# Performance work log

Measured on AMD Instinct MI355X. Metric: run time of the kernel, lower is better.

The kernel has to match this reference:

```python
import jax, jax.numpy as jnp
import numpy as np

B, L, D_IN, D_MODEL, D_STATE, D_DISCR, KER = 2, 1024, 512, 1024, 16, 64, 4


def setup_inputs() -> dict:
    ks = jax.random.split(jax.random.key(0), 9)
    s = 0.02
    return {
        "seq": jax.random.normal(ks[0], (B, L, D_IN), jnp.float32),
        "W_in": jax.random.normal(ks[1], (2 * D_MODEL, D_IN), jnp.float32) * s,
        "W_out": jax.random.normal(ks[2], (D_IN, D_MODEL), jnp.float32) * s,
        "W_B": jax.random.normal(ks[3], (D_STATE, D_MODEL), jnp.float32) * s,
        "W_C": jax.random.normal(ks[4], (D_STATE, D_MODEL), jnp.float32) * s,
        "W_D1": jax.random.normal(ks[5], (D_DISCR, D_MODEL), jnp.float32) * s,
        "W_D2": jax.random.normal(ks[6], (D_MODEL, D_DISCR), jnp.float32) * s,
        "conv_w": jax.random.normal(ks[7], (D_MODEL, 1, KER), jnp.float32) * 0.1,
        "conv_b": jax.random.normal(ks[8], (D_MODEL,), jnp.float32) * 0.01,
        "A": jnp.tile(jnp.arange(1, D_STATE + 1, dtype=jnp.float32), (D_MODEL, 1)),
        "D": jnp.ones((D_MODEL,), jnp.float32),
    }


def _causal_depthwise_conv(x, w, b):
    # x: [B, L, D] -> torch Conv1d(groups=D, padding=KER-1) truncated to first L outputs
    x = jnp.swapaxes(x, 1, 2)  # [B, D, L]
    y = jax.lax.conv_general_dilated(
        x, w, window_strides=(1,), padding=[(KER - 1, 0)],
        dimension_numbers=("NCH", "OIH", "NCH"), feature_group_count=D_MODEL)
    y = y + b[None, :, None]
    return jnp.swapaxes(y, 1, 2)  # [B, L, D]


def _ssm(x, W_B, W_C, W_D1, W_D2, A, D):
    # x: [B, L, D]
    exp_negA = jnp.exp(-A)                                  # [D, S]
    Bm = jnp.einsum("bld,sd->bls", x, W_B)                  # [B, L, S]
    Cm = jnp.einsum("bld,sd->bls", x, W_C)                  # [B, L, S]
    delta = jax.nn.softplus(D + jnp.einsum("ble,de->bld", jnp.einsum("bld,ed->ble", x, W_D1), W_D2))  # [B, L, D]
    A_bar = exp_negA[None, None] * delta[..., None]         # [B, L, D, S]
    X = Bm[:, :, None, :] * delta[..., None] * x[..., None]  # [B, L, D, S]

    def comb(c1, c2):
        a1, x1 = c1
        a2, x2 = c2
        return a1 * a2, a2 * x1 + x2

    _, h = jax.lax.associative_scan(comb, (A_bar, X), axis=1)  # h: [B, L, D, S]
    y = jnp.einsum("blds,bls->bld", h, Cm)
    return y + D * x


def reference(seq, W_in, W_out, W_B, W_C, W_D1, W_D2, conv_w, conv_b, A, D):
    ab = jnp.einsum("bli,oi->blo", seq, W_in)   # [B, L, 2*D_MODEL]
    a, b = ab[..., :D_MODEL], ab[..., D_MODEL:]
    a = jax.nn.silu(_causal_depthwise_conv(a, conv_w, conv_b))
    a = _ssm(a, W_B, W_C, W_D1, W_D2, A, D)
    out = a * jax.nn.silu(b)
    return jnp.einsum("bld,od->blo", out, W_out)  # [B, L, D_IN]
```

## Files before the change

kernel.cpp:

```cpp
#include <hip/hip_runtime.h>
#include <hip/hip_bf16.h>

typedef short short8 __attribute__((ext_vector_type(8)));
typedef short short4v __attribute__((ext_vector_type(4)));
typedef float float4v __attribute__((ext_vector_type(4)));

#define B_   2
#define L_   1024
#define DIN  512
#define DM   1024
#define DS   16
#define DD   64
#define KER_ 4
#define NROW (B_*L_)

#define SD   4
#define SC   128
#define SLC  8
#define NSEG 8

__device__ __forceinline__ float silu_f(float v){ return v / (1.f + expf(-v)); }

__device__ __forceinline__ short2 f2bf2(float a, float b) {
  __hip_bfloat162 h = __float22bfloat162_rn(float2{a, b});
  union { __hip_bfloat162 h; short2 s; } u; u.h = h; return u.s;
}
__device__ __forceinline__ short f2bf1(float a) {
  __hip_bfloat16 h = __float2bfloat16(a);
  union { __hip_bfloat16 h; short s; } u; u.h = h; return u.s;
}
__device__ __forceinline__ short8 pack8(const float4& x0, const float4& x1) {
  short2 s0 = f2bf2(x0.x, x0.y), s1 = f2bf2(x0.z, x0.w);
  short2 s2 = f2bf2(x1.x, x1.y), s3 = f2bf2(x1.z, x1.w);
  return short8{ s0.x, s0.y, s1.x, s1.y, s2.x, s2.y, s3.x, s3.y };
}
__device__ __forceinline__ float bf2f(short s) {
  union { unsigned u; float f; } v; v.u = ((unsigned)(unsigned short)s) << 16; return v.f;
}

__global__ __launch_bounds__(256)
void gemm1_k(const float* __restrict__ seq, const float* __restrict__ Win,
             __hip_bfloat16* __restrict__ ab, float* __restrict__ pall) {
  __shared__ short As[64 * 40];
  __shared__ short Bs[64 * 40];
  const int tid  = threadIdx.x;
  {
    int zi = (blockIdx.y * 32 + blockIdx.x) * 256 + tid;
    if (zi < NROW * 96) pall[zi] = 0.f;
  }
  const int lane = tid & 63;
  const int wave = tid >> 6;
  const int r16  = lane & 15;
  const int quad = lane >> 4;
  const int m0 = blockIdx.y * 64;
  const int n0 = blockIdx.x * 64;
  const int wm = wave & 1, wn = wave >> 1;
  float4v acc[2][2];
#pragma unroll
  for (int i = 0; i < 2; i++)
#pragma unroll
    for (int j = 0; j < 2; j++) acc[i][j] = (float4v){0.f, 0.f, 0.f, 0.f};
  float4 pf0[2], pf1[2];
  auto ldu = [&](int j, int k0) {
    int u = tid + j * 256;
    const float4* p;
    if (u < 256) { int row = u >> 2, q = u & 3;
      p = (const float4*)(seq + (size_t)(m0 + row) * DIN + k0 + q * 8);
    } else { int v = u - 256; int row = v >> 2, q = v & 3;
      p = (const float4*)(Win + (size_t)(n0 + row) * DIN + k0 + q * 8);
    }
    pf0[j] = p[0]; pf1[j] = p[1];
  };
  auto stu = [&](int j) {
    int u = tid + j * 256;
    short8 s = pack8(pf0[j], pf1[j]);
    if (u < 256) { int row = u >> 2, q = u & 3; *(short8*)&As[row * 40 + q * 8] = s; }
    else { int v = u - 256; int row = v >> 2, q = v & 3; *(short8*)&Bs[row * 40 + q * 8] = s; }
  };
  ldu(0, 0); ldu(1, 0);
  for (int k0 = 0; k0 < DIN; k0 += 32) {
    stu(0); stu(1);
    __syncthreads();
    if (k0 + 32 < DIN) { ldu(0, k0 + 32); ldu(1, k0 + 32); }
    short8 afr[2], bfr[2];
#pragma unroll
    for (int mi = 0; mi < 2; mi++)
      afr[mi] = *(const short8*)&As[(wm * 32 + mi * 16 + r16) * 40 + quad * 8];
#pragma unroll
    for (int ni = 0; ni < 2; ni++)
      bfr[ni] = *(const short8*)&Bs[(wn * 32 + ni * 16 + r16) * 40 + quad * 8];
#pragma unroll
    for (int mi = 0; mi < 2; mi++)
#pragma unroll
      for (int ni = 0; ni < 2; ni++)
        acc[mi][ni] = __builtin_amdgcn_mfma_f32_16x16x32_bf16(afr[mi], bfr[ni], acc[mi][ni], 0, 0, 0);
    __syncthreads();
  }
#pragma unroll
  for (int mi = 0; mi < 2; mi++)
#pragma unroll
    for (int ni = 0; ni < 2; ni++) {
      int gn = n0 + wn * 32 + ni * 16 + r16;
#pragma unroll
      for (int r = 0; r < 4; r++) {
        int gm = m0 + wm * 32 + mi * 16 + quad * 4 + r;
        ab[(size_t)gm * (2 * DM) + gn] = __float2bfloat16(acc[mi][ni][r]);
      }
    }
}

__global__ __launch_bounds__(256)
void convproj_k(const __hip_bfloat16* __restrict__ ab, const float* __restrict__ cw,
                const float* __restrict__ cb, const float* __restrict__ WB,
                const float* __restrict__ WC, const float* __restrict__ WD1,
                float* __restrict__ xt, short* __restrict__ gt,
                float* __restrict__ pall) {
  __shared__ char smraw[12800];
  const int blk = blockIdx.x;
  const int tid = threadIdx.x;

  if (blk < 1024) {
    short* tile = (short*)smraw;
    const int n0 = (blk & 31) * 64;
    const int d0 = (blk >> 5) * 64;
    const int l0 = n0 & (L_ - 1);
    for (int u = tid; u < 67 * 8; u += 256) {
      int r = u >> 3, c8 = u & 7;
      int l = l0 - 3 + r;
      short8 v = short8{0, 0, 0, 0, 0, 0, 0, 0};
      if (l >= 0 && r < 67)
        v = *(const short8*)(ab + (size_t)(n0 - l0 + l) * (2 * DM) + d0 + c8 * 8);
      *(short8*)&tile[r * 74 + c8 * 8] = v;
    }
    __syncthreads();
    const int i  = tid & 63;
    const int dl = tid >> 6;
    if (d0 < DM) {
#pragma unroll 4
      for (int p = 0; p < 16; p++) {
        int dc = p * 4 + dl;
        int d  = d0 + dc;
        float4 w = *(const float4*)(cw + d * 4);
        float a = cb[d];
        a += bf2f(tile[(i + 0) * 74 + dc]) * w.x;
        a += bf2f(tile[(i + 1) * 74 + dc]) * w.y;
        a += bf2f(tile[(i + 2) * 74 + dc]) * w.z;
        a += bf2f(tile[(i + 3) * 74 + dc]) * w.w;
        xt[(size_t)d * NROW + n0 + i] = silu_f(a);
      }
    } else {
#pragma unroll 4
      for (int p = 0; p < 16; p++) {
        int dc = p * 4 + dl;
        gt[(size_t)(d0 - DM + dc) * NROW + n0 + i] = tile[(i + 3) * 74 + dc];
      }
    }
    return;
  }

  short* As = (short*)smraw;
  short* Bs = As + 64 * 40;
  const int b2   = blk - 1024;
  const int lane = tid & 63;
  const int wave = tid >> 6;
  const int r16  = lane & 15;
  const int quad = lane >> 4;
  const int m0   = (b2 & 31) * 64;
  const int kbeg = (b2 >> 5) * 128;
  float4v acc[6];
#pragma unroll
  for (int i = 0; i < 6; i++) acc[i] = (float4v){0.f, 0.f, 0.f, 0.f};

  short8 ta[KER_];
  float4 pf0[2], pf1[2];
  const int arow = tid >> 2, aq = tid & 3;
  const int an = m0 + arow, al = an & (L_ - 1), abq = an >> 10;

  auto ldu_a = [&](int k0) {
#pragma unroll
    for (int t = 0; t < KER_; t++) {
      int ll = al - (KER_ - 1) + t;
      if (ll >= 0)
        ta[t] = *(const short8*)(ab + (size_t)(abq * L_ + ll) * (2 * DM) + k0 + aq * 8);
      else
        ta[t] = short8{0, 0, 0, 0, 0, 0, 0, 0};
    }
  };
  auto stu_a = [&](int k0) {
    float r8[8];
#pragma unroll
    for (int e = 0; e < 8; e++) {
      int d = k0 + aq * 8 + e;
      float4 w = *(const float4*)(cw + d * 4);
      float a = cb[d];
      a += bf2f(ta[0][e]) * w.x;
      a += bf2f(ta[1][e]) * w.y;
      a += bf2f(ta[2][e]) * w.z;
      a += bf2f(ta[3][e]) * w.w;
      r8[e] = silu_f(a);
    }
    *(short8*)&As[arow * 40 + aq * 8] =
        pack8(float4{r8[0], r8[1], r8[2], r8[3]}, float4{r8[4], r8[5], r8[6], r8[7]});
  };
  auto ldu_b = [&](int j, int k0) {
    int u = tid + j * 256;
    if (u >= 640) return;
    int v = u - 256, row = v >> 2, q = v & 3;
    const float* bp = (row < 16) ? (WB + (size_t)row * DM)
                    : (row < 32) ? (WC + (size_t)(row - 16) * DM)
                                 : (WD1 + (size_t)(row - 32) * DM);
    const float4* p = (const float4*)(bp + k0 + q * 8);
    pf0[j - 1] = p[0]; pf1[j - 1] = p[1];
  };
  auto stu_b = [&](int j) {
    int u = tid + j * 256;
    if (u >= 640) return;
    int v = u - 256, row = v >> 2, q = v & 3;
    *(short8*)&Bs[row * 40 + q * 8] = pack8(pf0[j - 1], pf1[j - 1]);
  };

  ldu_a(kbeg); ldu_b(1, kbeg); ldu_b(2, kbeg);
  for (int k0 = kbeg; k0 < kbeg + 128; k0 += 32) {
    stu_a(k0); stu_b(1); stu_b(2);
    __syncthreads();
    if (k0 + 32 < kbeg + 128) { ldu_a(k0 + 32); ldu_b(1, k0 + 32); ldu_b(2, k0 + 32); }
    short8 afr = *(const short8*)&As[(wave * 16 + r16) * 40 + quad * 8];
#pragma unroll
    for (int ni = 0; ni < 6; ni++) {
      short8 bfr = *(const short8*)&Bs[(ni * 16 + r16) * 40 + quad * 8];
      acc[ni] = __builtin_amdgcn_mfma_f32_16x16x32_bf16(afr, bfr, acc[ni], 0, 0, 0);
    }
    __syncthreads();
  }
#pragma unroll
  for (int ni = 0; ni < 6; ni++) {
    int gn = ni * 16 + r16;
#pragma unroll
    for (int r = 0; r < 4; r++) {
      int gm = m0 + wave * 16 + quad * 4 + r;
      atomicAdd(&pall[(size_t)gm * 96 + gn], acc[ni][r]);
    }
  }
}

__global__ __launch_bounds__(256)
void delta_k(const float* __restrict__ t1, const float* __restrict__ WD2,
             const float* __restrict__ Dv, float* __restrict__ dltT) {
  __shared__ short As[64 * 40];
  __shared__ short Bs[64 * 40];
  const int tid  = threadIdx.x;
  const int lane = tid & 63;
  const int wave = tid >> 6;
  const int r16  = lane & 15;
  const int quad = lane >> 4;
  const int m0 = blockIdx.y * 64;
  const int n0 = blockIdx.x * 64;
  const int wm = wave & 1, wn = wave >> 1;
  float4v acc[2][2];
#pragma unroll
  for (int i = 0; i < 2; i++)
#pragma unroll
    for (int j = 0; j < 2; j++) acc[i][j] = (float4v){0.f, 0.f, 0.f, 0.f};
  float4 pf0[2], pf1[2];
  auto ldu = [&](int j, int k0) {
    int u = tid + j * 256;
    const float4* p;
    if (u < 256) { int row = u >> 2, q = u & 3;
      p = (const float4*)(t1 + (size_t)(m0 + row) * 96 + k0 + q * 8);
    } else { int v = u - 256; int row = v >> 2, q = v & 3;
      p = (const float4*)(WD2 + (size_t)(n0 + row) * DD + k0 + q * 8);
    }
    pf0[j] = p[0]; pf1[j] = p[1];
  };
  auto stu = [&](int j) {
    int u = tid + j * 256;
    short8 s = pack8(pf0[j], pf1[j]);
    if (u < 256) { int row = u >> 2, q = u & 3; *(short8*)&As[row * 40 + q * 8] = s; }
    else { int v = u - 256; int row = v >> 2, q = v & 3; *(short8*)&Bs[row * 40 + q * 8] = s; }
  };
  ldu(0, 0); ldu(1, 0);
  for (int k0 = 0; k0 < DD; k0 += 32) {
    stu(0); stu(1);
    __syncthreads();
    if (k0 + 32 < DD) { ldu(0, k0 + 32); ldu(1, k0 + 32); }
    short8 afr[2], bfr[2];
#pragma unroll
    for (int mi = 0; mi < 2; mi++)
      afr[mi] = *(const short8*)&As[(wm * 32 + mi * 16 + r16) * 40 + quad * 8];
#pragma unroll
    for (int ni = 0; ni < 2; ni++)
      bfr[ni] = *(const short8*)&Bs[(wn * 32 + ni * 16 + r16) * 40 + quad * 8];
#pragma unroll
    for (int mi = 0; mi < 2; mi++)
#pragma unroll
      for (int ni = 0; ni < 2; ni++)
        acc[mi][ni] = __builtin_amdgcn_mfma_f32_16x16x32_bf16(afr[mi], bfr[ni], acc[mi][ni], 0, 0, 0);
    __syncthreads();
  }
#pragma unroll
  for (int mi = 0; mi < 2; mi++)
#pragma unroll
    for (int ni = 0; ni < 2; ni++) {
      int gn = n0 + wn * 32 + ni * 16 + r16;
      float dvn = Dv[gn];
#pragma unroll
      for (int r = 0; r < 4; r++) {
        int gm = m0 + wm * 32 + mi * 16 + quad * 4 + r;
        float v = acc[mi][ni][r] + dvn;
        v = fmaxf(v, 0.f) + log1pf(expf(-fabsf(v)));
        dltT[(size_t)gn * NROW + gm] = v;
      }
    }
}

__global__ __launch_bounds__(512, 2)
void scan_fused_k(const float* __restrict__ xt, const float* __restrict__ dltT,
                  const float* __restrict__ pall, const float* __restrict__ A,
                  const float* __restrict__ Dv, const short* __restrict__ gt,
                  short* __restrict__ soutb) {
  __shared__ float Pl[DS * SD][SC + 1];
  __shared__ float Hl[DS * SD][SC + 1];
  __shared__ float Ps[DS * SD][NSEG + 1];
  __shared__ float Hs[DS * SD][NSEG + 1];
  const int blk = blockIdx.x;
  const int b   = blk >> 8;
  const int d0  = (blk & 255) * SD;
  const int dd  = threadIdx.x & (SD - 1);
  const int c   = threadIdx.x >> 2;
  const int d   = d0 + dd;

  float e[DS];
#pragma unroll
  for (int s = 0; s < DS; s++) e[s] = expf(-A[d * DS + s]);

  const int nbase = b * L_ + c * SLC;
  const float* xrow = xt   + (size_t)d * NROW;
  const float* drow = dltT + (size_t)d * NROW;
  const short* grow = gt   + (size_t)d * NROW;

  float h[DS];
#pragma unroll
  for (int s = 0; s < DS; s++) h[s] = 0.f;
  float pdl = 1.f;
#pragma unroll
  for (int q = 0; q < SLC / 4; q++) {
    const int n = nbase + q * 4;
    float4 x4 = *(const float4*)(xrow + n);
    float4 d4 = *(const float4*)(drow + n);
    float4 bq[4][4];
#pragma unroll
    for (int t = 0; t < 4; t++) {
      const float4* pp = (const float4*)(pall + (size_t)(n + t) * 96);
      bq[t][0] = pp[0]; bq[t][1] = pp[1]; bq[t][2] = pp[2]; bq[t][3] = pp[3];
    }
#pragma unroll
    for (int t = 0; t < 4; t++) {
      float dl = (&d4.x)[t], xv = (&x4.x)[t];
      float dx = dl * xv;
      pdl *= dl;
      float bmv[DS] = { bq[t][0].x, bq[t][0].y, bq[t][0].z, bq[t][0].w,
                        bq[t][1].x, bq[t][1].y, bq[t][1].z, bq[t][1].w,
                        bq[t][2].x, bq[t][2].y, bq[t][2].z, bq[t][2].w,
                        bq[t][3].x, bq[t][3].y, bq[t][3].z, bq[t][3].w };
#pragma unroll
      for (int s = 0; s < DS; s++)
        h[s] = (e[s] * dl) * h[s] + bmv[s] * dx;
    }
  }
#pragma unroll
  for (int s = 0; s < DS; s++) {
    float e2 = e[s] * e[s], e4 = e2 * e2, e8 = e4 * e4;
    Pl[dd * DS + s][c] = e8 * pdl;
    Hl[dd * DS + s][c] = h[s];
  }
  __syncthreads();

  {
    const int seg = threadIdx.x >> 6;
    const int cmb = threadIdx.x & 63;
    float* Prow = &Pl[cmb][0];
    float* Hrow = &Hl[cmb][0];
    float Pa = 1.f, Ha = 0.f;
#pragma unroll
    for (int i = 0; i < SC / NSEG; i++) {
      int c2 = seg * (SC / NSEG) + i;
      float p = Prow[c2], hh = Hrow[c2];
      Prow[c2] = Pa;
      Hrow[c2] = Ha;
      Ha = p * Ha + hh;
      Pa *= p;
    }
    Ps[cmb][seg] = Pa;
    Hs[cmb][seg] = Ha;
  }
  __syncthreads();

  if (threadIdx.x < DS * SD) {
    float* Pr = &Ps[threadIdx.x][0];
    float* Hr = &Hs[threadIdx.x][0];
    float H = 0.f;
#pragma unroll
    for (int g = 0; g < NSEG; g++) {
      float p = Pr[g], hh = Hr[g];
      Hr[g] = H;
      H = p * H + hh;
    }
  }
  __syncthreads();

  {
    const int g = c >> 4;
#pragma unroll
    for (int s = 0; s < DS; s++)
      h[s] = Pl[dd * DS + s][c] * Hs[dd * DS + s][g] + Hl[dd * DS + s][c];
  }
  const float Dd = Dv[d];
#pragma unroll
  for (int q = 0; q < SLC / 4; q++) {
    const int n = nbase + q * 4;
    float4 x4 = *(const float4*)(xrow + n);
    float4 d4 = *(const float4*)(drow + n);
    short4v g4 = *(const short4v*)(grow + n);
    float4 bq[4][4], cq[4][4];
#pragma unroll
    for (int t = 0; t < 4; t++) {
      const float4* pp = (const float4*)(pall + (size_t)(n + t) * 96);
      bq[t][0] = pp[0]; bq[t][1] = pp[1]; bq[t][2] = pp[2]; bq[t][3] = pp[3];
      cq[t][0] = pp[4]; cq[t][1] = pp[5]; cq[t][2] = pp[6]; cq[t][3] = pp[7];
    }
#pragma unroll
    for (int t = 0; t < 4; t++) {
      float dl = (&d4.x)[t], xv = (&x4.x)[t];
      float dx = dl * xv;
      float bmv[DS] = { bq[t][0].x, bq[t][0].y, bq[t][0].z, bq[t][0].w,
                        bq[t][1].x, bq[t][1].y, bq[t][1].z, bq[t][1].w,
                        bq[t][2].x, bq[t][2].y, bq[t][2].z, bq[t][2].w,
                        bq[t][3].x, bq[t][3].y, bq[t][3].z, bq[t][3].w };
      float cmv[DS] = { cq[t][0].x, cq[t][0].y, cq[t][0].z, cq[t][0].w,
                        cq[t][1].x, cq[t][1].y, cq[t][1].z, cq[t][1].w,
                        cq[t][2].x, cq[t][2].y, cq[t][2].z, cq[t][2].w,
                        cq[t][3].x, cq[t][3].y, cq[t][3].z, cq[t][3].w };
      float y = 0.f;
#pragma unroll
      for (int s = 0; s < DS; s++) {
        h[s] = (e[s] * dl) * h[s] + bmv[s] * dx;
        y += h[s] * cmv[s];
      }
      y += Dd * xv;
      float gg = bf2f(g4[t]);
      soutb[(size_t)(n + t) * DM + d] = f2bf1(y * silu_f(gg));
    }
  }
}

__global__ __launch_bounds__(256)
void gemm2_k(const short* __restrict__ soutb, const float* __restrict__ Wout,
             float* __restrict__ out) {
  __shared__ short As[64 * 40];
  __shared__ short Bs[32 * 40];
  const int tid  = threadIdx.x;
  const int lane = tid & 63;
  const int wave = tid >> 6;
  const int r16  = lane & 15;
  const int quad = lane >> 4;
  const int m0 = blockIdx.y * 64;
  const int n0 = blockIdx.x * 32;
  const int wm = wave & 1, wn = wave >> 1;
  float4v acc[2];
  acc[0] = (float4v){0.f, 0.f, 0.f, 0.f};
  acc[1] = (float4v){0.f, 0.f, 0.f, 0.f};
  short8 pa;
  float4 pf0, pf1;
  auto ldu = [&](int k0) {
    {
      int row = tid >> 2, q = tid & 3;
      pa = *(const short8*)(soutb + (size_t)(m0 + row) * DM + k0 + q * 8);
    }
    if (tid < 128) {
      int row = tid >> 2, q = tid & 3;
      const float4* p = (const float4*)(Wout + (size_t)(n0 + row) * DM + k0 + q * 8);
      pf0 = p[0]; pf1 = p[1];
    }
  };
  auto stu = [&]() {
    { int row = tid >> 2, q = tid & 3; *(short8*)&As[row * 40 + q * 8] = pa; }
    if (tid < 128) { int row = tid >> 2, q = tid & 3; *(short8*)&Bs[row * 40 + q * 8] = pack8(pf0, pf1); }
  };
  ldu(0);
  for (int k0 = 0; k0 < DM; k0 += 32) {
    stu();
    __syncthreads();
    if (k0 + 32 < DM) ldu(k0 + 32);
    short8 afr[2], bfr;
    afr[0] = *(const short8*)&As[(wm * 32 + r16) * 40 + quad * 8];
    afr[1] = *(const short8*)&As[(wm * 32 + 16 + r16) * 40 + quad * 8];
    bfr    = *(const short8*)&Bs[(wn * 16 + r16) * 40 + quad * 8];
    acc[0] = __builtin_amdgcn_mfma_f32_16x16x32_bf16(afr[0], bfr, acc[0], 0, 0, 0);
    acc[1] = __builtin_amdgcn_mfma_f32_16x16x32_bf16(afr[1], bfr, acc[1], 0, 0, 0);
    __syncthreads();
  }
#pragma unroll
  for (int mi = 0; mi < 2; mi++)
#pragma unroll
    for (int r = 0; r < 4; r++)
      out[(size_t)(m0 + wm * 32 + mi * 16 + quad * 4 + r) * DIN + n0 + wn * 16 + r16] = acc[mi][r];
}

extern "C" void kernel_launch(void* const* d_in, const int* in_sizes, int n_in,
                              void* d_out, int out_size, void* d_ws, size_t ws_size,
                              hipStream_t stream) {
  const float* seq  = (const float*)d_in[0];
  const float* Win  = (const float*)d_in[1];
  const float* Wout = (const float*)d_in[2];
  const float* WB   = (const float*)d_in[3];
  const float* WC   = (const float*)d_in[4];
  const float* WD1  = (const float*)d_in[5];
  const float* WD2  = (const float*)d_in[6];
  const float* cw   = (const float*)d_in[7];
  const float* cb   = (const float*)d_in[8];
  const float* A    = (const float*)d_in[9];
  const float* Dv   = (const float*)d_in[10];
  float* out = (float*)d_out;

  float* ws = (float*)d_ws;
  __hip_bfloat16* ab = (__hip_bfloat16*)ws;
  float* xt   = ws   + 2097152;
  short* gt   = (short*)(xt + 2097152);
  float* dltT = (float*)(gt + 2097152);
  float* pall = dltT + 2097152;
  short* soutb = (short*)(pall + 196608);
  float* t1   = pall + 32;

  gemm1_k<<<dim3(32, 32), 256, 0, stream>>>(seq, Win, ab, pall);
  convproj_k<<<1280, 256, 0, stream>>>(ab, cw, cb, WB, WC, WD1, xt, gt, pall);
  delta_k<<<dim3(16, 32), 256, 0, stream>>>(t1, WD2, Dv, dltT);
  scan_fused_k<<<B_ * (DM / SD), 512, 0, stream>>>(xt, dltT, pall, A, Dv, gt, soutb);
  gemm2_k<<<dim3(16, 32), 256, 0, stream>>>(soutb, Wout, out);
}
```

Baseline: 162.1 us.

## Enlarge gemm1 tiles to 128x128 and vectorize conv tile LDS reads

The input-projection GEMM now uses 128x128 output tiles with 512 threads, 8 waves each owning a 64x32 subtile. This raises operand reuse and shrinks the grid from 1024 to 256 blocks, with the zeroing of pall adjusted to match. The conv kernel pads the LDS tile to 72 shorts per row and reads 8 channels at once as short8 instead of scalar shorts, cutting LDS instructions. The risks are fewer blocks than the GPU's 256 CUs can fully use, higher register use, and possible new bank conflicts from the new row stride.

```diff
diff --git a/kernel.cpp b/kernel.cpp
--- a/kernel.cpp
+++ b/kernel.cpp
@@ -38,72 +38,68 @@
   union { unsigned u; float f; } v; v.u = ((unsigned)(unsigned short)s) << 16; return v.f;
 }
 
-__global__ __launch_bounds__(256)
+__global__ __launch_bounds__(512)
 void gemm1_k(const float* __restrict__ seq, const float* __restrict__ Win,
              __hip_bfloat16* __restrict__ ab, float* __restrict__ pall) {
-  __shared__ short As[64 * 40];
-  __shared__ short Bs[64 * 40];
+  __shared__ short As[128 * 40];
+  __shared__ short Bs[128 * 40];
   const int tid  = threadIdx.x;
   {
-    int zi = (blockIdx.y * 32 + blockIdx.x) * 256 + tid;
-    if (zi < NROW * 96) pall[zi] = 0.f;
+    int zi = (blockIdx.y * 16 + blockIdx.x) * 1024 + tid * 2;
+    if (zi < NROW * 96) { pall[zi] = 0.f; pall[zi + 1] = 0.f; }
   }
   const int lane = tid & 63;
   const int wave = tid >> 6;
   const int r16  = lane & 15;
   const int quad = lane >> 4;
-  const int m0 = blockIdx.y * 64;
-  const int n0 = blockIdx.x * 64;
-  const int wm = wave & 1, wn = wave >> 1;
-  float4v acc[2][2];
-#pragma unroll
-  for (int i = 0; i < 2; i++)
+  const int m0 = blockIdx.y * 128;
+  const int n0 = blockIdx.x * 128;
+  const int wm = wave & 1;
+  const int wn = wave >> 1;
+  float4v acc[4][2];
+#pragma unroll
+  for (int i = 0; i < 4; i++)
 #pragma unroll
     for (int j = 0; j < 2; j++) acc[i][j] = (float4v){0.f, 0.f, 0.f, 0.f};
-  float4 pf0[2], pf1[2];
-  auto ldu = [&](int j, int k0) {
-    int u = tid + j * 256;
-    const float4* p;
-    if (u < 256) { int row = u >> 2, q = u & 3;
-      p = (const float4*)(seq + (size_t)(m0 + row) * DIN + k0 + q * 8);
-    } else { int v = u - 256; int row = v >> 2, q = v & 3;
-      p = (const float4*)(Win + (size_t)(n0 + row) * DIN + k0 + q * 8);
-    }
-    pf0[j] = p[0]; pf1[j] = p[1];
-  };
-  auto stu = [&](int j) {
-    int u = tid + j * 256;
-    short8 s = pack8(pf0[j], pf1[j]);
-    if (u < 256) { int row = u >> 2, q = u & 3; *(short8*)&As[row * 40 + q * 8] = s; }
-    else { int v = u - 256; int row = v >> 2, q = v & 3; *(short8*)&Bs[row * 40 + q * 8] = s; }
-  };
-  ldu(0, 0); ldu(1, 0);
+  const int row = tid >> 2, q = tid & 3;
+  float4 pfA0, pfA1, pfB0, pfB1;
+  auto ldu = [&](int k0) {
+    const float4* pa = (const float4*)(seq + (size_t)(m0 + row) * DIN + k0 + q * 8);
+    pfA0 = pa[0]; pfA1 = pa[1];
+    const float4* pb = (const float4*)(Win + (size_t)(n0 + row) * DIN + k0 + q * 8);
+    pfB0 = pb[0]; pfB1 = pb[1];
+  };
+  auto stu = [&]() {
+    *(short8*)&As[row * 40 + q * 8] = pack8(pfA0, pfA1);
+    *(short8*)&Bs[row * 40 + q * 8] = pack8(pfB0, pfB1);
+  };
+  ldu(0);
   for (int k0 = 0; k0 < DIN; k0 += 32) {
-    stu(0); stu(1);
-    __syncthreads();
-    if (k0 + 32 < DIN) { ldu(0, k0 + 32); ldu(1, k0 + 32); }
-    short8 afr[2], bfr[2];
-#pragma unroll
-    for (int mi = 0; mi < 2; mi++)
-      afr[mi] = *(const short8*)&As[(wm * 32 + mi * 16 + r16) * 40 + quad * 8];
+    stu();
+    __syncthreads();
+    if (k0 + 32 < DIN) ldu(k0 + 32);
+    short8 afr[4], bfr[2];
+#pragma unroll
+    for (int mi = 0; mi < 4; mi++)
+      afr[mi] = *(const short8*)&As[(wm * 64 + mi * 16 + r16) * 40 + quad * 8];
 #pragma unroll
     for (int ni = 0; ni < 2; ni++)
       bfr[ni] = *(const short8*)&Bs[(wn * 32 + ni * 16 + r16) * 40 + quad * 8];
 #pragma unroll
-    for (int mi = 0; mi < 2; mi++)
+    for (int mi = 0; mi < 4; mi++)
 #pragma unroll
       for (int ni = 0; ni < 2; ni++)
         acc[mi][ni] = __builtin_amdgcn_mfma_f32_16x16x32_bf16(afr[mi], bfr[ni], acc[mi][ni], 0, 0, 0);
     __syncthreads();
   }
 #pragma unroll
-  for (int mi = 0; mi < 2; mi++)
+  for (int mi = 0; mi < 4; mi++)
 #pragma unroll
     for (int ni = 0; ni < 2; ni++) {
       int gn = n0 + wn * 32 + ni * 16 + r16;
 #pragma unroll
       for (int r = 0; r < 4; r++) {
-        int gm = m0 + wm * 32 + mi * 16 + quad * 4 + r;
+        int gm = m0 + wm * 64 + mi * 16 + quad * 4 + r;
         ab[(size_t)gm * (2 * DM) + gn] = __float2bfloat16(acc[mi][ni][r]);
       }
     }
@@ -130,29 +126,39 @@
       short8 v = short8{0, 0, 0, 0, 0, 0, 0, 0};
       if (l >= 0 && r < 67)
         v = *(const short8*)(ab + (size_t)(n0 - l0 + l) * (2 * DM) + d0 + c8 * 8);
-      *(short8*)&tile[r * 74 + c8 * 8] = v;
+      *(short8*)&tile[r * 72 + c8 * 8] = v;
     }
     __syncthreads();
     const int i  = tid & 63;
     const int dl = tid >> 6;
     if (d0 < DM) {
-#pragma unroll 4
-      for (int p = 0; p < 16; p++) {
-        int dc = p * 4 + dl;
-        int d  = d0 + dc;
-        float4 w = *(const float4*)(cw + d * 4);
-        float a = cb[d];
-        a += bf2f(tile[(i + 0) * 74 + dc]) * w.x;
-        a += bf2f(tile[(i + 1) * 74 + dc]) * w.y;
-        a += bf2f(tile[(i + 2) * 74 + dc]) * w.z;
-        a += bf2f(tile[(i + 3) * 74 + dc]) * w.w;
-        xt[(size_t)d * NROW + n0 + i] = silu_f(a);
+#pragma unroll
+      for (int p8 = 0; p8 < 2; p8++) {
+        const int dc0 = dl * 16 + p8 * 8;
+        short8 t0 = *(const short8*)&tile[(i + 0) * 72 + dc0];
+        short8 t1 = *(const short8*)&tile[(i + 1) * 72 + dc0];
+        short8 t2 = *(const short8*)&tile[(i + 2) * 72 + dc0];
+        short8 t3 = *(const short8*)&tile[(i + 3) * 72 + dc0];
+#pragma unroll
+        for (int e = 0; e < 8; e++) {
+          int d = d0 + dc0 + e;
+          float4 w = *(const float4*)(cw + d * 4);
+          float a = cb[d];
+          a += bf2f(t0[e]) * w.x;
+          a += bf2f(t1[e]) * w.y;
+          a += bf2f(t2[e]) * w.z;
+          a += bf2f(t3[e]) * w.w;
+          xt[(size_t)d * NROW + n0 + i] = silu_f(a);
+        }
       }
     } else {
-#pragma unroll 4
-      for (int p = 0; p < 16; p++) {
-        int dc = p * 4 + dl;
-        gt[(size_t)(d0 - DM + dc) * NROW + n0 + i] = tile[(i + 3) * 74 + dc];
+#pragma unroll
+      for (int p8 = 0; p8 < 2; p8++) {
+        const int dc0 = dl * 16 + p8 * 8;
+        short8 v = *(const short8*)&tile[(i + 3) * 72 + dc0];
+#pragma unroll
+        for (int e = 0; e < 8; e++)
+          gt[(size_t)(d0 - DM + dc0 + e) * NROW + n0 + i] = v[e];
       }
     }
     return;
@@ -531,7 +537,7 @@
   short* soutb = (short*)(pall + 196608);
   float* t1   = pall + 32;
 
-  gemm1_k<<<dim3(32, 32), 256, 0, stream>>>(seq, Win, ab, pall);
+  gemm1_k<<<dim3(16, 16), 512, 0, stream>>>(seq, Win, ab, pall);
   convproj_k<<<1280, 256, 0, stream>>>(ab, cw, cb, WB, WC, WD1, xt, gt, pall);
   delta_k<<<dim3(16, 32), 256, 0, stream>>>(t1, WD2, Dv, dltT);
   scan_fused_k<<<B_ * (DM / SD), 512, 0, stream>>>(xt, dltT, pall, A, Dv, gt, soutb);
```

Result: no change. 161.1 us (-0.6%).
